# Kernel tuning notes

Measured on AMD Instinct MI355X. Metric: run time of the kernel, lower is better.

## Reference

```python
import jax, jax.numpy as jnp
import numpy as np

B, S, D = 8, 4096, 1024
H, DH = 16, 64
DM = H * DH  # d_model = 1024


def setup_inputs() -> dict:
    key = jax.random.key(0)
    k0, k1, k2, k3 = jax.random.split(key, 4)
    x = jax.random.uniform(k0, (B, S, D), dtype=jnp.float32)
    # nn.Linear weights (stored here pre-transposed as [in, out]).
    Wq = jax.random.normal(k1, (D, DM), dtype=jnp.float32) * 0.02
    Wkv = jax.random.normal(k2, (D, 2 * DM), dtype=jnp.float32) * 0.02
    Wlin = jax.random.normal(k3, (DM, DM), dtype=jnp.float32) * 0.02
    blin = jnp.zeros((DM,), dtype=jnp.float32)
    return {"x": x, "Wq": Wq, "Wkv": Wkv, "Wlin": Wlin, "blin": blin}


def reference(x, Wq, Wkv, Wlin, blin):
    scale = DH ** (-0.5)
    # projections; cond_dim=None => cond = x (self attention), mask=None
    q = (x @ Wq).reshape(B, S, H, DH)          # [B,S,H,DH]
    kv = (x @ Wkv).reshape(B, S, H, 2 * DH)    # [B,S,H,2*DH]
    k, v = kv[..., :DH], kv[..., DH:]
    # dual softmax: q over feature dim (scaled), k over sequence dim
    q = jax.nn.softmax(q, axis=-1) * scale
    k = jax.nn.softmax(k, axis=1)              # seq axis in BSHD layout
    # context = k^T @ v per (batch, head): [B,H,DH,DH]
    context = jnp.einsum('bshd,bshe->bhde', k, v)
    # out = q @ context: [B,S,H,DH]
    out = jnp.einsum('bshd,bhde->bshe', q, context).reshape(B, S, DM)
    return out @ Wlin + blin
```

## Files before the change

### kernel.cpp

```cpp
#include <hip/hip_runtime.h>
#include <hip/hip_bf16.h>
#include <cstdint>

using bf16 = __hip_bfloat16;
typedef __attribute__((ext_vector_type(8))) short bf16x8;
typedef __attribute__((ext_vector_type(4))) float f32x4;

struct alignas(16) B8 { bf16 h[8]; };
struct alignas(8)  B4 { bf16 h[4]; };

__device__ __forceinline__ void gll16(const void* g, void* l) {
  __builtin_amdgcn_global_load_lds((__attribute__((address_space(1))) void*)g,
                                   (__attribute__((address_space(3))) void*)l,
                                   16, 0, 0);
}

__global__ void cast_f32_bf16(const float* __restrict__ in, bf16* __restrict__ out, long long n) {
  long long i = ((long long)blockIdx.x * blockDim.x + threadIdx.x) * 8;
  if (i >= n) return;
  float4 v0 = *(const float4*)(in + i);
  float4 v1 = *(const float4*)(in + i + 4);
  B8 o;
  o.h[0] = __float2bfloat16(v0.x); o.h[1] = __float2bfloat16(v0.y);
  o.h[2] = __float2bfloat16(v0.z); o.h[3] = __float2bfloat16(v0.w);
  o.h[4] = __float2bfloat16(v1.x); o.h[5] = __float2bfloat16(v1.y);
  o.h[6] = __float2bfloat16(v1.z); o.h[7] = __float2bfloat16(v1.w);
  *(B8*)(out + i) = o;
}

__global__ void tcast(const float* __restrict__ W, bf16* __restrict__ WT, int K, int N) {
  __shared__ float tile[32][33];
  int k0 = blockIdx.y * 32, n0 = blockIdx.x * 32;
  int tx = threadIdx.x, ty = threadIdx.y;
  for (int yy = ty; yy < 32; yy += 8)
    tile[yy][tx] = W[(size_t)(k0 + yy) * N + n0 + tx];
  __syncthreads();
  for (int yy = ty; yy < 32; yy += 8)
    WT[(size_t)(n0 + yy) * K + k0 + tx] = __float2bfloat16(tile[tx][yy]);
}

__device__ __forceinline__ void gemm_mainloop_256(
    const bf16* __restrict__ aop0, const bf16* __restrict__ aop1,
    const bf16* __restrict__ bop0, const bf16* __restrict__ bop1,
    bf16* ldsA, bf16* ldsB, int wd0, int wd1,
    int arow, int brow, int fc, f32x4 (&acc)[8][4])
{
#define STAGE_A(slot, ko) do { gll16(aop0 + (ko), ldsA + (slot) * 8192 + wd0); \
                               gll16(aop1 + (ko), ldsA + (slot) * 8192 + wd1); } while (0)
#define STAGE_B(slot, ko) do { gll16(bop0 + (ko), ldsB + (slot) * 8192 + wd0); \
                               gll16(bop1 + (ko), ldsB + (slot) * 8192 + wd1); } while (0)
#define AFRAG(slot, i) (*(const bf16x8*)(ldsA + (slot) * 8192 + (arow + (i) * 16) * 32 + fc))
#define BFRAG(slot, j) (*(const bf16x8*)(ldsB + (slot) * 8192 + (brow + (j) * 16) * 32 + fc))

  STAGE_A(0, 0); STAGE_B(0, 0);
  STAGE_A(1, 32); STAGE_B(1, 32);

  #pragma unroll 2
  for (int kt = 0; kt < 16; ++kt) {
    const bool more = kt < 15;
    #pragma unroll
    for (int h = 0; h < 2; ++h) {
      const int sh = (2 * kt + h) & 3;
      const int ph = (2 * kt + 2 + h) & 3;
      const int ko = (kt + 1) * 64 + h * 32;

      if (more || h == 0) { asm volatile("s_waitcnt vmcnt(4)" ::: "memory"); }
      else               { asm volatile("s_waitcnt vmcnt(0)" ::: "memory"); }
      __builtin_amdgcn_s_barrier();
      __builtin_amdgcn_sched_barrier(0);

      if (more) STAGE_A(ph, ko);

      bf16x8 a[4], b[4];
      #pragma unroll
      for (int j = 0; j < 4; j++) b[j] = BFRAG(sh, j);
      #pragma unroll
      for (int i = 0; i < 4; i++) a[i] = AFRAG(sh, i);
      asm volatile("s_waitcnt lgkmcnt(0)" ::: "memory");
      __builtin_amdgcn_sched_barrier(0);

      __builtin_amdgcn_s_setprio(1);
      #pragma unroll
      for (int i = 0; i < 4; i++) {
        #pragma unroll
        for (int j = 0; j < 4; j++)
          acc[i][j] = __builtin_amdgcn_mfma_f32_16x16x32_bf16(a[i], b[j], acc[i][j], 0, 0, 0);
        a[i] = AFRAG(sh, i + 4);
      }
      __builtin_amdgcn_s_setprio(0);

      if (more) STAGE_B(ph, ko);
      asm volatile("s_waitcnt lgkmcnt(0)" ::: "memory");
      __builtin_amdgcn_sched_barrier(0);

      __builtin_amdgcn_s_setprio(1);
      #pragma unroll
      for (int i = 0; i < 4; i++)
        #pragma unroll
        for (int j = 0; j < 4; j++)
          acc[i + 4][j] = __builtin_amdgcn_mfma_f32_16x16x32_bf16(a[i], b[j], acc[i + 4][j], 0, 0, 0);
      __builtin_amdgcn_s_setprio(0);
    }
  }
  __syncthreads();
#undef STAGE_A
#undef STAGE_B
#undef AFRAG
#undef BFRAG
}

constexpr int QKV_NT = 12;

__global__ __launch_bounds__(512, 2)
void gemm_qkv(const bf16* __restrict__ A, const bf16* __restrict__ BT,
              bf16* __restrict__ Yq, float* __restrict__ ctxAcc)
{
  __shared__ __align__(16) union {
    struct { bf16 a[4 * 8192]; bf16 b[4 * 8192]; } g;
    struct { bf16 ekT[2][16384]; bf16 vT[2][16384]; } c;
  } sm;

  const int t = threadIdx.x;
  const int wave = t >> 6, lane = t & 63;
  const int lr = lane & 15, kq = lane >> 4;
  const int wm = wave >> 2, wn = wave & 3;
  const int bid = (int)blockIdx.x;
  const int swz = (bid & 7) * 192 + (bid >> 3);
  const int bm = swz / QKV_NT, bn = swz % QKV_NT;
  const int m0 = bm * 256, n0 = bn * 256;

  const int srow = t >> 2;
  const int cl = (t & 3) ^ ((srow ^ (srow >> 2)) & 3);
  const bf16* aop0 = A + (size_t)(m0 + srow) * 1024 + cl * 8;
  const bf16* aop1 = A + (size_t)(m0 + 128 + srow) * 1024 + cl * 8;
  const bf16* bop0 = BT + (size_t)(n0 + srow) * 1024 + cl * 8;
  const bf16* bop1 = BT + (size_t)(n0 + 128 + srow) * 1024 + cl * 8;
  const int wd0 = wave * 512;
  const int wd1 = 4096 + wave * 512;

  const int fc = (kq ^ ((lr ^ (lr >> 2)) & 3)) * 8;
  const int arow = wm * 128 + lr;
  const int brow = wn * 64 + lr;

  const f32x4 zero = {0.f, 0.f, 0.f, 0.f};
  f32x4 acc[8][4];
  #pragma unroll
  for (int i = 0; i < 8; i++)
    #pragma unroll
    for (int j = 0; j < 4; j++) acc[i][j] = zero;

  gemm_mainloop_256(aop0, aop1, bop0, bop1, sm.g.a, sm.g.b, wd0, wd1,
                    arow, brow, fc, acc);

  if (bn < 4) {
    #pragma unroll
    for (int i = 0; i < 8; i++) {
      #pragma unroll
      for (int r = 0; r < 4; r++) {
        float m = fmaxf(fmaxf(acc[i][0][r], acc[i][1][r]),
                        fmaxf(acc[i][2][r], acc[i][3][r]));
        m = fmaxf(m, __shfl_xor(m, 1));
        m = fmaxf(m, __shfl_xor(m, 2));
        m = fmaxf(m, __shfl_xor(m, 4));
        m = fmaxf(m, __shfl_xor(m, 8));
        float ex[4]; float s = 0.f;
        #pragma unroll
        for (int j = 0; j < 4; j++) { ex[j] = __expf(acc[i][j][r] - m); s += ex[j]; }
        s += __shfl_xor(s, 1);
        s += __shfl_xor(s, 2);
        s += __shfl_xor(s, 4);
        s += __shfl_xor(s, 8);
        const float inv = 0.125f / s;
        const int row = m0 + wm * 128 + i * 16 + kq * 4 + r;
        bf16* yrow = Yq + (size_t)row * 1024 + n0 + wn * 64;
        #pragma unroll
        for (int j = 0; j < 4; j++)
          yrow[j * 16 + lr] = __float2bfloat16(ex[j] * inv);
      }
    }
  } else {
    const int bb = m0 >> 12;
    const int h0 = (n0 - 1024) >> 7;
    const int hloc = wn >> 1, isV = wn & 1;
    bf16* const dstT = (isV ? sm.c.vT[hloc] : sm.c.ekT[hloc]);

    float zp[4] = {0.f, 0.f, 0.f, 0.f};
    #pragma unroll
    for (int i = 0; i < 8; i++) {
      const int sbase = wm * 128 + i * 16 + kq * 4;
      const int sxo = sbase >> 3;
      const int sby = (sbase & 7) * 2;
      #pragma unroll
      for (int j = 0; j < 4; j++) {
        const int d = j * 16 + lr;
        B4 pk;
        if (!isV) {
          #pragma unroll
          for (int r = 0; r < 4; r++) {
            float e = __expf(acc[i][j][r]);
            zp[j] += e;
            pk.h[r] = __float2bfloat16(e);
          }
        } else {
          #pragma unroll
          for (int r = 0; r < 4; r++) pk.h[r] = __float2bfloat16(acc[i][j][r]);
        }
        *(B4*)((char*)dstT + d * 512 + ((sxo ^ (d & 7)) << 4) + sby) = pk;
      }
    }

    if (!isV) {
      #pragma unroll
      for (int j = 0; j < 4; j++) {
        zp[j] += __shfl_xor(zp[j], 16);
        zp[j] += __shfl_xor(zp[j], 32);
      }
      if (kq == 0) {
        float* zb = ctxAcc + (size_t)(bb * 16 + h0 + hloc) * 4160 + 4096;
        #pragma unroll
        for (int j = 0; j < 4; j++) atomicAdd(zb + j * 16 + lr, zp[j]);
      }
    }
    __syncthreads();

    const int hh = wave >> 2, dq = wave & 3;
    const bf16* const ek = sm.c.ekT[hh];
    const bf16* const vv = sm.c.vT[hh];
    f32x4 racc[4] = {zero, zero, zero, zero};
    #pragma unroll
    for (int ks = 0; ks < 8; ks++) {
      const int ch = ks * 4 + kq;
      bf16x8 af = *(const bf16x8*)((const char*)ek + (dq * 16 + lr) * 512 + ((ch ^ (lr & 7)) << 4));
      #pragma unroll
      for (int j = 0; j < 4; j++) {
        bf16x8 bfr = *(const bf16x8*)((const char*)vv + (j * 16 + lr) * 512 + ((ch ^ (lr & 7)) << 4));
        racc[j] = __builtin_amdgcn_mfma_f32_16x16x32_bf16(af, bfr, racc[j], 0, 0, 0);
      }
    }
    float* cb = ctxAcc + (size_t)(bb * 16 + h0 + hh) * 4160;
    #pragma unroll
    for (int j = 0; j < 4; j++) {
      #pragma unroll
      for (int r = 0; r < 4; r++)
        atomicAdd(cb + (dq * 16 + kq * 4 + r) * 64 + j * 16 + lr, racc[j][r]);
    }
  }
}

__global__ __launch_bounds__(256) void make_w2t(const float* __restrict__ ctxAcc,
                                                const bf16* __restrict__ WlinT,
                                                bf16* __restrict__ W2T) {
  const int nc = blockIdx.x;
  const int bh = blockIdx.y;
  const int b = bh >> 4, h = bh & 15;
  const int t = threadIdx.x, lane = t & 63, w = t >> 6;
  const float* src = ctxAcc + (size_t)bh * 4160;
  const float invz = 1.0f / src[4096 + lane];
  float creg[64];
  const float* crow = src + lane * 64;
  #pragma unroll
  for (int e4 = 0; e4 < 16; e4++) {
    float4 v = *(const float4*)(crow + e4 * 4);
    creg[e4 * 4 + 0] = v.x * invz; creg[e4 * 4 + 1] = v.y * invz;
    creg[e4 * 4 + 2] = v.z * invz; creg[e4 * 4 + 3] = v.w * invz;
  }
  for (int i = 0; i < 16; i++) {
    const int n = nc * 64 + w * 16 + i;
    const bf16* wrow = WlinT + (size_t)n * 1024 + h * 64;
    float acc = 0.f;
    #pragma unroll
    for (int e8 = 0; e8 < 8; e8++) {
      B8 v = *(const B8*)(wrow + e8 * 8);
      #pragma unroll
      for (int j = 0; j < 8; j++) acc += creg[e8 * 8 + j] * __bfloat162float(v.h[j]);
    }
    W2T[((size_t)b * 1024 + n) * 1024 + h * 64 + lane] = __float2bfloat16(acc);
  }
}

__global__ __launch_bounds__(512, 2)
void gemm_out(const bf16* __restrict__ Aall, const bf16* __restrict__ BTall,
              float* __restrict__ Call, const float* __restrict__ bias)
{
  __shared__ __align__(16) struct { bf16 a[4 * 8192]; bf16 b[4 * 8192]; } sm;
  const int t = threadIdx.x;
  const int wave = t >> 6, lane = t & 63;
  const int lr = lane & 15, kq = lane >> 4;
  const int wm = wave >> 2, wn = wave & 3;
  const int bid = (int)blockIdx.x;
  const int swz = (bid & 7) * 64 + (bid >> 3);
  const int bz = swz >> 6;
  const int r  = swz & 63;
  const int bm = r >> 2, bn = r & 3;
  const int m0 = bm * 256, n0 = bn * 256;
  const bf16* A  = Aall  + (size_t)bz * 4096 * 1024;
  const bf16* BT = BTall + (size_t)bz * 1024 * 1024;
  float* C       = Call  + (size_t)bz * 4096 * 1024;

  const int srow = t >> 2;
  const int cl = (t & 3) ^ ((srow ^ (srow >> 2)) & 3);
  const bf16* aop0 = A + (size_t)(m0 + srow) * 1024 + cl * 8;
  const bf16* aop1 = A + (size_t)(m0 + 128 + srow) * 1024 + cl * 8;
  const bf16* bop0 = BT + (size_t)(n0 + srow) * 1024 + cl * 8;
  const bf16* bop1 = BT + (size_t)(n0 + 128 + srow) * 1024 + cl * 8;
  const int wd0 = wave * 512;
  const int wd1 = 4096 + wave * 512;

  const int fc = (kq ^ ((lr ^ (lr >> 2)) & 3)) * 8;
  const int arow = wm * 128 + lr;
  const int brow = wn * 64 + lr;

  const f32x4 zero = {0.f, 0.f, 0.f, 0.f};
  f32x4 acc[8][4];
  #pragma unroll
  for (int i = 0; i < 8; i++)
    #pragma unroll
    for (int j = 0; j < 4; j++) acc[i][j] = zero;

  gemm_mainloop_256(aop0, aop1, bop0, bop1, sm.a, sm.b, wd0, wd1,
                    arow, brow, fc, acc);

  float bv[4];
  #pragma unroll
  for (int j = 0; j < 4; j++) bv[j] = bias[n0 + wn * 64 + j * 16 + lr];
  #pragma unroll
  for (int i = 0; i < 8; i++) {
    const int row0 = m0 + wm * 128 + i * 16 + kq * 4;
    #pragma unroll
    for (int j = 0; j < 4; j++) {
      const int col = n0 + wn * 64 + j * 16 + lr;
      const float bvj = bv[j];
      #pragma unroll
      for (int r2 = 0; r2 < 4; r2++)
        C[(size_t)(row0 + r2) * 1024 + col] = acc[i][j][r2] + bvj;
    }
  }
}

extern "C" void kernel_launch(void* const* d_in, const int* in_sizes, int n_in,
                              void* d_out, int out_size, void* d_ws, size_t ws_size,
                              hipStream_t stream) {
  (void)in_sizes; (void)n_in; (void)out_size; (void)ws_size;
  const float* x    = (const float*)d_in[0];
  const float* Wq   = (const float*)d_in[1];
  const float* Wkv  = (const float*)d_in[2];
  const float* Wlin = (const float*)d_in[3];
  const float* blin = (const float*)d_in[4];
  float* out = (float*)d_out;

  bf16* x_bf  = (bf16*)d_ws;
  bf16* WTc   = x_bf + 33554432;
  bf16* WlinT = WTc + 3145728;
  bf16* Yq    = WlinT + 1048576;
  bf16* W2T   = Yq + 33554432;
  float* ctxAcc = (float*)(W2T + 8388608);

  cast_f32_bf16<<<16384, 256, 0, stream>>>(x, x_bf, 33554432LL);
  tcast<<<dim3(32, 32), dim3(32, 8), 0, stream>>>(Wq, WTc, 1024, 1024);
  tcast<<<dim3(64, 32), dim3(32, 8), 0, stream>>>(Wkv, WTc + 1048576, 1024, 2048);
  tcast<<<dim3(32, 32), dim3(32, 8), 0, stream>>>(Wlin, WlinT, 1024, 1024);

  hipMemsetAsync(ctxAcc, 0, (size_t)128 * 4160 * sizeof(float), stream);

  gemm_qkv<<<dim3(128 * QKV_NT), 512, 0, stream>>>(x_bf, WTc, Yq, ctxAcc);
  make_w2t<<<dim3(16, 128), 256, 0, stream>>>(ctxAcc, WlinT, W2T);
  gemm_out<<<dim3(512), 512, 0, stream>>>(Yq, W2T, out, blin);
}
```

Before: 390.8 us.

## Software-pipeline GEMM mainloop with register-prefetched fragments and deeper LDS staging

Restructures the bf16 GEMM mainloop so the A and B fragments for the next K-slice are read from LDS into double-buffered registers while the current MFMAs run. All four LDS slots are now kept in flight, with A and B staged together at each barrier. The loop is manually unrolled into 4-slot sections with explicit vmcnt waits. This aims to hide LDS read latency and barrier stalls behind MFMA work, at the cost of extra registers under the 512-thread, 2-block launch bound and more complex wait accounting.

```diff
diff --git a/kernel.cpp b/kernel.cpp
--- a/kernel.cpp
+++ b/kernel.cpp
@@ -52,57 +52,76 @@
 #define AFRAG(slot, i) (*(const bf16x8*)(ldsA + (slot) * 8192 + (arow + (i) * 16) * 32 + fc))
 #define BFRAG(slot, j) (*(const bf16x8*)(ldsB + (slot) * 8192 + (brow + (j) * 16) * 32 + fc))
 
-  STAGE_A(0, 0); STAGE_B(0, 0);
+  bf16x8 a1[4], a2[4], bb[2][4];
+
+#define SECTION(S, CURB, NXTB, DO_PF, PFS)                                          \
+  do {                                                                              \
+    asm volatile("s_waitcnt lgkmcnt(0)" ::: "memory");                              \
+    __builtin_amdgcn_sched_barrier(0);                                              \
+    __builtin_amdgcn_s_setprio(1);                                                  \
+    _Pragma("unroll")                                                               \
+    for (int i = 0; i < 4; i++) {                                                   \
+      _Pragma("unroll")                                                             \
+      for (int j = 0; j < 4; j++)                                                   \
+        acc[i][j] = __builtin_amdgcn_mfma_f32_16x16x32_bf16(a1[i], bb[CURB][j],     \
+                                                            acc[i][j], 0, 0, 0);    \
+      a2[i] = AFRAG(S, i + 4);                                                      \
+    }                                                                               \
+    asm volatile("s_waitcnt lgkmcnt(0)" ::: "memory");                              \
+    __builtin_amdgcn_sched_barrier(0);                                              \
+    _Pragma("unroll")                                                               \
+    for (int i = 0; i < 4; i++) {                                                   \
+      _Pragma("unroll")                                                             \
+      for (int j = 0; j < 4; j++)                                                   \
+        acc[i + 4][j] = __builtin_amdgcn_mfma_f32_16x16x32_bf16(a2[i], bb[CURB][j], \
+                                                                acc[i + 4][j], 0, 0, 0); \
+      if (DO_PF) { bb[NXTB][i] = BFRAG(PFS, i); a1[i] = AFRAG(PFS, i); }            \
+    }                                                                               \
+    __builtin_amdgcn_s_setprio(0);                                                  \
+  } while (0)
+
+#define BOUNDARY(VMC, DO_STAGE, SLOT, KO)                                           \
+  do {                                                                              \
+    asm volatile("s_waitcnt vmcnt(" #VMC ")" ::: "memory");                         \
+    __builtin_amdgcn_s_barrier();                                                   \
+    __builtin_amdgcn_sched_barrier(0);                                              \
+    if (DO_STAGE) { STAGE_A(SLOT, KO); STAGE_B(SLOT, KO); }                         \
+  } while (0)
+
+  STAGE_A(0, 0);  STAGE_B(0, 0);
   STAGE_A(1, 32); STAGE_B(1, 32);
-
-  #pragma unroll 2
-  for (int kt = 0; kt < 16; ++kt) {
-    const bool more = kt < 15;
-    #pragma unroll
-    for (int h = 0; h < 2; ++h) {
-      const int sh = (2 * kt + h) & 3;
-      const int ph = (2 * kt + 2 + h) & 3;
-      const int ko = (kt + 1) * 64 + h * 32;
-
-      if (more || h == 0) { asm volatile("s_waitcnt vmcnt(4)" ::: "memory"); }
-      else               { asm volatile("s_waitcnt vmcnt(0)" ::: "memory"); }
-      __builtin_amdgcn_s_barrier();
-      __builtin_amdgcn_sched_barrier(0);
-
-      if (more) STAGE_A(ph, ko);
-
-      bf16x8 a[4], b[4];
-      #pragma unroll
-      for (int j = 0; j < 4; j++) b[j] = BFRAG(sh, j);
-      #pragma unroll
-      for (int i = 0; i < 4; i++) a[i] = AFRAG(sh, i);
-      asm volatile("s_waitcnt lgkmcnt(0)" ::: "memory");
-      __builtin_amdgcn_sched_barrier(0);
-
-      __builtin_amdgcn_s_setprio(1);
-      #pragma unroll
-      for (int i = 0; i < 4; i++) {
-        #pragma unroll
-        for (int j = 0; j < 4; j++)
-          acc[i][j] = __builtin_amdgcn_mfma_f32_16x16x32_bf16(a[i], b[j], acc[i][j], 0, 0, 0);
-        a[i] = AFRAG(sh, i + 4);
-      }
-      __builtin_amdgcn_s_setprio(0);
-
-      if (more) STAGE_B(ph, ko);
-      asm volatile("s_waitcnt lgkmcnt(0)" ::: "memory");
-      __builtin_amdgcn_sched_barrier(0);
-
-      __builtin_amdgcn_s_setprio(1);
-      #pragma unroll
-      for (int i = 0; i < 4; i++)
-        #pragma unroll
-        for (int j = 0; j < 4; j++)
-          acc[i + 4][j] = __builtin_amdgcn_mfma_f32_16x16x32_bf16(a[i], b[j], acc[i + 4][j], 0, 0, 0);
-      __builtin_amdgcn_s_setprio(0);
-    }
-  }
+  STAGE_A(2, 64); STAGE_B(2, 64);
+  asm volatile("s_waitcnt vmcnt(8)" ::: "memory");
+  __builtin_amdgcn_s_barrier();
+  __builtin_amdgcn_sched_barrier(0);
+  STAGE_A(3, 96); STAGE_B(3, 96);
+  #pragma unroll
+  for (int j = 0; j < 4; j++) bb[0][j] = BFRAG(0, j);
+  #pragma unroll
+  for (int i = 0; i < 4; i++) a1[i] = AFRAG(0, i);
+
+  for (int q = 0; q < 7; ++q) {
+    const int ko = q * 128 + 128;
+    SECTION(0, 0, 1, true, 1);
+    BOUNDARY(4, true, 0, ko);
+    SECTION(1, 1, 0, true, 2);
+    BOUNDARY(4, true, 1, ko + 32);
+    SECTION(2, 0, 1, true, 3);
+    BOUNDARY(4, true, 2, ko + 64);
+    SECTION(3, 1, 0, true, 0);
+    BOUNDARY(4, true, 3, ko + 96);
+  }
+  SECTION(0, 0, 1, true, 1);
+  BOUNDARY(4, false, 0, 0);
+  SECTION(1, 1, 0, true, 2);
+  BOUNDARY(0, false, 0, 0);
+  SECTION(2, 0, 1, true, 3);
+  BOUNDARY(0, false, 0, 0);
+  SECTION(3, 1, 0, false, 0);
+
   __syncthreads();
+#undef SECTION
+#undef BOUNDARY
 #undef STAGE_A
 #undef STAGE_B
 #undef AFRAG
@@ -179,7 +198,7 @@
       }
     }
   } else {
-    const int bb = m0 >> 12;
+    const int bb2 = m0 >> 12;
     const int h0 = (n0 - 1024) >> 7;
     const int hloc = wn >> 1, isV = wn & 1;
     bf16* const dstT = (isV ? sm.c.vT[hloc] : sm.c.ekT[hloc]);
@@ -216,7 +235,7 @@
         zp[j] += __shfl_xor(zp[j], 32);
       }
       if (kq == 0) {
-        float* zb = ctxAcc + (size_t)(bb * 16 + h0 + hloc) * 4160 + 4096;
+        float* zb = ctxAcc + (size_t)(bb2 * 16 + h0 + hloc) * 4160 + 4096;
         #pragma unroll
         for (int j = 0; j < 4; j++) atomicAdd(zb + j * 16 + lr, zp[j]);
       }
@@ -237,7 +256,7 @@
         racc[j] = __builtin_amdgcn_mfma_f32_16x16x32_bf16(af, bfr, racc[j], 0, 0, 0);
       }
     }
-    float* cb = ctxAcc + (size_t)(bb * 16 + h0 + hh) * 4160;
+    float* cb = ctxAcc + (size_t)(bb2 * 16 + h0 + hh) * 4160;
     #pragma unroll
     for (int j = 0; j < 4; j++) {
       #pragma unroll
```

Result: no change. 389.8 us (-0.2%).
